# Performance work log

Hardware: AMD Instinct MI355X
Metric: run time of the kernel (lower is better)

## Reference

```python
import jax, jax.numpy as jnp
import numpy as np

T, B, D_IN = 1024, 64, 17
H_MAIN = 150   # per-direction hidden of main bi-GRU (hidden_dim=300)
H_HIER = 128   # per-direction hidden of hier bi-GRU (hier_hidden=256)
M = 16         # uniform measure length (eoM fires every M steps)
N_MEAS = T // M
N_PITCH, N_KS = 35, 15
PAD_P, PAD_K = 34, 14


def _gru(x, Wih, Whh, bih, bhh):
    # x: [T, N, D]; torch GRU gate order is (r, z, n)
    H = Whh.shape[1]
    gi_all = jnp.einsum('tnd,gd->tng', x, Wih) + bih  # input-side gates, precomputed

    def step(h, gi):
        gh = h @ Whh.T + bhh
        ir, iz, inn = jnp.split(gi, 3, axis=-1)
        hr, hz, hn = jnp.split(gh, 3, axis=-1)
        r = jax.nn.sigmoid(ir + hr)
        z = jax.nn.sigmoid(iz + hz)
        n = jnp.tanh(inn + r * hn)
        h_new = (1.0 - z) * n + z * h
        return h_new, h_new

    h0 = jnp.zeros((x.shape[1], H), x.dtype)
    _, ys = jax.lax.scan(step, h0, gi_all)
    return ys


def _bigru(x, pf, pb):
    yf = _gru(x, *pf)
    yb = _gru(x[::-1], *pb)[::-1]
    return jnp.concatenate([yf, yb], axis=-1)


def _ce(logits, targets, pad_idx):
    # mean cross-entropy with ignore_index=pad_idx
    logp = jax.nn.log_softmax(logits, axis=-1)
    mask = (targets != pad_idx).astype(logits.dtype)
    nll = -jnp.take_along_axis(logp, targets[:, None], axis=1)[:, 0]
    return jnp.sum(nll * mask) / jnp.maximum(jnp.sum(mask), 1.0)


def _forward(sentences, mWih_f, mWhh_f, mbih_f, mbhh_f, mWih_b, mWhh_b, mbih_b, mbhh_b,
             hWih_f, hWhh_f, hbih_f, hbhh_f, hWih_b, hWhh_b, hbih_b, hbhh_b,
             Wq, bq, Wv, bv, Wp, bp, Wk, bk, pitches, keysignatures):
    # main bi-GRU over full sequences: [T, B, 300]
    rnn_out = _bigru(sentences, (mWih_f, mWhh_f, mbih_f, mbhh_f),
                     (mWih_b, mWhh_b, mbih_b, mbhh_b))
    H2 = rnn_out.shape[-1]
    # carve uniform measures: [T,B,H2] -> [M, B*N_MEAS, H2]
    seg = rnn_out.reshape(N_MEAS, M, B, H2).transpose(1, 2, 0, 3).reshape(M, B * N_MEAS, H2)
    hier = _bigru(seg, (hWih_f, hWhh_f, hbih_f, hbhh_f),
                  (hWih_b, hWhh_b, hbih_b, hbhh_b))  # [M, B*N_MEAS, 256]
    HH = hier.shape[-1]
    # attention per measure: query = value = hier outputs [B*N_MEAS, M, 256]
    hv = hier.reshape(M, B, N_MEAS, HH).transpose(1, 2, 0, 3).reshape(B * N_MEAS, M, HH)
    q = hv @ Wq.T + bq
    v = hv @ Wv.T + bv
    attn = jax.nn.softmax(jnp.einsum('nld,nmd->nlm', q, v), axis=-1)
    ctx = jnp.einsum('nlm,nmd->nd', attn, hv).reshape(B, N_MEAS, HH)  # sum over l of attn@value
    # repeat each measure context over its M timesteps: [T, B, 256]
    ctx_t = jnp.repeat(ctx, M, axis=1).transpose(1, 0, 2)
    stacked = jnp.concatenate([rnn_out, ctx_t], axis=-1)  # [T, B, 556]
    out_pitch = stacked @ Wp.T + bp   # [T, B, 35]
    out_ks = ctx_t @ Wk.T + bk        # [T, B, 15]
    return (_ce(out_pitch.reshape(-1, N_PITCH), pitches.reshape(-1), PAD_P)
            + _ce(out_ks.reshape(-1, N_KS), keysignatures.reshape(-1), PAD_K))


def setup_inputs() -> dict:
    key = jax.random.key(0)
    ks = jax.random.split(key, 32)

    def w(i, *shape):
        return jax.random.normal(ks[i], shape, jnp.float32) * 0.05

    G_M, G_H = 3 * H_MAIN, 3 * H_HIER
    inp = {
        'sentences': jax.random.normal(ks[0], (T, B, D_IN), jnp.float32),
        'pitches': jax.random.randint(ks[1], (T, B), 0, PAD_P),
        'keysignatures': jax.random.randint(ks[2], (T, B), 0, PAD_K),
        'sentences_len': jnp.full((B,), T, dtype=jnp.int32),
        'eoM': jnp.tile(((jnp.arange(T) % M) == M - 1).astype(jnp.int32)[:, None], (1, B)),
        'mWih_f': w(3, G_M, D_IN), 'mWhh_f': w(4, G_M, H_MAIN), 'mbih_f': w(5, G_M), 'mbhh_f': w(6, G_M),
        'mWih_b': w(7, G_M, D_IN), 'mWhh_b': w(8, G_M, H_MAIN), 'mbih_b': w(9, G_M), 'mbhh_b': w(10, G_M),
        'hWih_f': w(11, G_H, 2 * H_MAIN), 'hWhh_f': w(12, G_H, H_HIER), 'hbih_f': w(13, G_H), 'hbhh_f': w(14, G_H),
        'hWih_b': w(15, G_H, 2 * H_MAIN), 'hWhh_b': w(16, G_H, H_HIER), 'hbih_b': w(17, G_H), 'hbhh_b': w(18, G_H),
        'Wq': w(19, 2 * H_HIER, 2 * H_HIER), 'bq': w(20, 2 * H_HIER),
        'Wv': w(21, 2 * H_HIER, 2 * H_HIER), 'bv': w(22, 2 * H_HIER),
        'Wp': w(23, N_PITCH, 2 * H_MAIN + 2 * H_HIER), 'bp': w(24, N_PITCH),
        'Wk': w(25, N_KS, 2 * H_HIER), 'bk': w(26, N_KS),
    }
    return inp


def reference(sentences, pitches, keysignatures, sentences_len, eoM,
              mWih_f, mWhh_f, mbih_f, mbhh_f, mWih_b, mWhh_b, mbih_b, mbhh_b,
              hWih_f, hWhh_f, hbih_f, hbhh_f, hWih_b, hWhh_b, hbih_b, hbhh_b,
              Wq, bq, Wv, bv, Wp, bp, Wk, bk):
    # sentences_len/eoM encode the (uniform) measure structure M=16, full lengths;
    # the segment layout is baked in statically, so they are structural constants here.
    return _forward(sentences, mWih_f, mWhh_f, mbih_f, mbhh_f, mWih_b, mWhh_b, mbih_b, mbhh_b,
                    hWih_f, hWhh_f, hbih_f, hbhh_f, hWih_b, hWhh_b, hbih_b, hbhh_b,
                    Wq, bq, Wv, bv, Wp, bp, Wk, bk, pitches, keysignatures)
```

## Files before the change

kernel.cpp:

```cpp
#include <hip/hip_runtime.h>
#include <cstddef>

constexpr int kT   = 1024;
constexpr int kB   = 64;
constexpr int kDIN = 17;
constexpr int kHM  = 150;
constexpr int kHH  = 128;
constexpr int kM   = 16;
constexpr int kD2  = 300;
constexpr int kNP  = 35;
constexpr int kNK  = 15;

constexpr size_t OFF_RNN16  = 0;
constexpr size_t OFF_HV16   = 10485760;
constexpr size_t OFF_PART   = 18894848;
constexpr size_t OFF_PTPACK = 19988480;
constexpr size_t OFF_U      = 20021248;
constexpr size_t OFF_W      = 20021504;
constexpr size_t OFF_C0     = 20021760;
constexpr size_t OFF_KSLOGP = 20021792;
constexpr size_t OFF_CLOG   = 20083232;
constexpr size_t OFF_BPACK  = 20318752;
constexpr size_t OFF_BPACKL = 20490784;

typedef __bf16 bf16x8 __attribute__((ext_vector_type(8)));
typedef float f32x4 __attribute__((ext_vector_type(4)));

__device__ __forceinline__ unsigned short f2bf(float f) {
  unsigned u = __float_as_uint(f);
  u += 0x7FFFu + ((u >> 16) & 1u);
  return (unsigned short)(u >> 16);
}
__device__ __forceinline__ float bf2f(unsigned short v) {
  return __uint_as_float(((unsigned)v) << 16);
}
__device__ __forceinline__ float sigm(float x) {
  return __builtin_amdgcn_rcpf(1.f + __expf(-x));
}
__device__ __forceinline__ float tanh_fast(float x) {
  return 1.f - 2.f * __builtin_amdgcn_rcpf(__expf(2.f * x) + 1.f);
}

__global__ __launch_bounds__(640, 2) void k_mega(
    const float* __restrict__ x,
    const float* __restrict__ mWih_f, const float* __restrict__ mWhh_f,
    const float* __restrict__ mWih_b, const float* __restrict__ mWhh_b,
    const float* __restrict__ mbih_f, const float* __restrict__ mbhh_f,
    const float* __restrict__ mbih_b, const float* __restrict__ mbhh_b,
    const float* __restrict__ hWih_f, const float* __restrict__ hWhh_f,
    const float* __restrict__ hWih_b, const float* __restrict__ hWhh_b,
    const float* __restrict__ Wp,
    const float* __restrict__ Wq, const float* __restrict__ bq,
    const float* __restrict__ Wv, const float* __restrict__ bv,
    unsigned short* __restrict__ rnn16,
    unsigned short* __restrict__ bpack,
    unsigned short* __restrict__ bpackL,
    unsigned short* __restrict__ pp,
    float* __restrict__ u, float* __restrict__ w,
    float* __restrict__ c0)
{
  __shared__ __align__(16) unsigned short hx[2][160];
  __shared__ __align__(16) unsigned short hist[2][16][160];
  __shared__ __align__(16) unsigned short xall[kT][32];
  const int blk = blockIdx.x;
  if (blk < 128) {
    const int d = blk & 1, b = blk >> 1;
    const int tid = threadIdx.x, wv = tid >> 6, lane = tid & 63;
    const int col = lane & 15, q8 = (lane >> 4) * 8;
    for (int i = tid; i < 2 * 160; i += 640) ((unsigned short*)hx)[i] = 0;
    for (int i = tid; i < 2 * 16 * 160; i += 640) ((unsigned short*)hist)[i] = 0;
    for (int i = tid; i < kT * 32; i += 640) {
      const int t = i >> 5, c = i & 31;
      xall[t][c] = (c < kDIN) ? f2bf(x[((size_t)t * kB + b) * kDIN + c])
                              : (unsigned short)0;
    }
    const float* bih = d ? mbih_b : mbih_f;
    const float* bhh = d ? mbhh_b : mbhh_f;
    const float* Wihd = d ? mWih_b : mWih_f;
    const float* Whhd = d ? mWhh_b : mWhh_f;
    const int j = wv * 16 + col;
    const bool actv = (lane < 16) && (j < kHM);
    float br = 0.f, bz = 0.f, bnx = 0.f, bnh = 0.f;
    if (actv) {
      br  = bih[j] + bhh[j];
      bz  = bih[150 + j] + bhh[150 + j];
      bnx = bih[300 + j];
      bnh = bhh[300 + j];
    }
    bf16x8 bw[3][6];
    const int gts[3] = { wv, 10 + wv, 20 + wv };
    const int kb = (lane >> 4) * 8;
#pragma unroll
    for (int gi = 0; gi < 3; gi++) {
      const int slot = gts[gi] * 16 + col;
      const int type = slot / 160, jh = slot - type * 160;
      const int row = type * 150 + jh;
      const bool valid = (jh < 150);
#pragma unroll
      for (int kt = 0; kt < 6; kt++) {
        union { bf16x8 v; unsigned short us[8]; } tmp;
        if (kt < 5) {
          const int k0 = kt * 32 + kb;
          if (valid && (k0 + 8 <= 150)) {
#pragma unroll
            for (int p = 0; p < 4; p++) {
              const float2 f2 = *(const float2*)&Whhd[row * 150 + k0 + 2 * p];
              tmp.us[2 * p]     = f2bf(f2.x);
              tmp.us[2 * p + 1] = f2bf(f2.y);
            }
          } else {
#pragma unroll
            for (int jj = 0; jj < 8; jj++) {
              const int k = k0 + jj;
              tmp.us[jj] = (valid && k < 150) ? f2bf(Whhd[row * 150 + k])
                                              : (unsigned short)0;
            }
          }
        } else {
#pragma unroll
          for (int jj = 0; jj < 8; jj++) {
            const int k = kb + jj;
            tmp.us[jj] = (valid && k < 17) ? f2bf(Wihd[row * 17 + k])
                                           : (unsigned short)0;
          }
        }
        bw[gi][kt] = tmp.v;
      }
    }
    float h_old = 0.f;
    __syncthreads();

    for (int t = 0; t < kT; t++) {
      const int tx = d ? (kT - 1 - t) : t;
      const int buf = t & 1;
      bf16x8 afr[6];
#pragma unroll
      for (int kt = 0; kt < 5; kt++) afr[kt] = *(const bf16x8*)&hx[buf][kt * 32 + q8];
      afr[5] = *(const bf16x8*)&xall[tx][q8];
      f32x4 aR0 = (f32x4)(0.f), aR1 = (f32x4)(0.f), aR2 = (f32x4)(0.f);
      f32x4 aZ0 = (f32x4)(0.f), aZ1 = (f32x4)(0.f), aZ2 = (f32x4)(0.f);
      f32x4 aN0 = (f32x4)(0.f), aN1 = (f32x4)(0.f), aN2 = (f32x4)(0.f);
      f32x4 aX  = (f32x4)(0.f);
      aR0 = __builtin_amdgcn_mfma_f32_16x16x32_bf16(afr[0], bw[0][0], aR0, 0, 0, 0);
      aZ0 = __builtin_amdgcn_mfma_f32_16x16x32_bf16(afr[0], bw[1][0], aZ0, 0, 0, 0);
      aN0 = __builtin_amdgcn_mfma_f32_16x16x32_bf16(afr[0], bw[2][0], aN0, 0, 0, 0);
      aR1 = __builtin_amdgcn_mfma_f32_16x16x32_bf16(afr[1], bw[0][1], aR1, 0, 0, 0);
      aZ1 = __builtin_amdgcn_mfma_f32_16x16x32_bf16(afr[1], bw[1][1], aZ1, 0, 0, 0);
      aN1 = __builtin_amdgcn_mfma_f32_16x16x32_bf16(afr[1], bw[2][1], aN1, 0, 0, 0);
      aR2 = __builtin_amdgcn_mfma_f32_16x16x32_bf16(afr[2], bw[0][2], aR2, 0, 0, 0);
      aZ2 = __builtin_amdgcn_mfma_f32_16x16x32_bf16(afr[2], bw[1][2], aZ2, 0, 0, 0);
      aN2 = __builtin_amdgcn_mfma_f32_16x16x32_bf16(afr[2], bw[2][2], aN2, 0, 0, 0);
      aR0 = __builtin_amdgcn_mfma_f32_16x16x32_bf16(afr[3], bw[0][3], aR0, 0, 0, 0);
      aZ0 = __builtin_amdgcn_mfma_f32_16x16x32_bf16(afr[3], bw[1][3], aZ0, 0, 0, 0);
      aN0 = __builtin_amdgcn_mfma_f32_16x16x32_bf16(afr[3], bw[2][3], aN0, 0, 0, 0);
      aR1 = __builtin_amdgcn_mfma_f32_16x16x32_bf16(afr[4], bw[0][4], aR1, 0, 0, 0);
      aZ1 = __builtin_amdgcn_mfma_f32_16x16x32_bf16(afr[4], bw[1][4], aZ1, 0, 0, 0);
      aN1 = __builtin_amdgcn_mfma_f32_16x16x32_bf16(afr[4], bw[2][4], aN1, 0, 0, 0);
      aR2 = __builtin_amdgcn_mfma_f32_16x16x32_bf16(afr[5], bw[0][5], aR2, 0, 0, 0);
      aZ2 = __builtin_amdgcn_mfma_f32_16x16x32_bf16(afr[5], bw[1][5], aZ2, 0, 0, 0);
      aX  = __builtin_amdgcn_mfma_f32_16x16x32_bf16(afr[5], bw[2][5], aX, 0, 0, 0);
      if (actv) {
        const float r = sigm(aR0[0] + aR1[0] + aR2[0] + br);
        const float z = sigm(aZ0[0] + aZ1[0] + aZ2[0] + bz);
        const float n = tanh_fast(aX[0] + bnx + r * (aN0[0] + aN1[0] + aN2[0] + bnh));
        h_old = (1.f - z) * n + z * h_old;
        const unsigned short us = f2bf(h_old);
        hx[buf ^ 1][j] = us;
        hist[(t >> 4) & 1][t & 15][j] = us;
      }
      __syncthreads();
      if ((t & 15) == 15) {
        const int hb = (t >> 4) & 1;
        const int toff = tid / 40, ch = tid - toff * 40;
        const int tg = t - 15 + toff;
        const int txg = d ? (kT - 1 - tg) : tg;
        *(ushort4*)&rnn16[((size_t)txg * kB + b) * 320 + d * 160 + ch * 4] =
            *(const ushort4*)&hist[hb][toff][ch * 4];
      }
    }
  } else if (blk < 199) {
    const int sub = threadIdx.x >> 6, lane = threadIdx.x & 63;
    int bid = (blk - 128) * 10 + sub;
    if (bid >= 702) return;
    if (bid < 672) {
      const int kt = bid % 14;
      const int nt = (bid / 14) % 24;
      const int d  = bid / (14 * 24);
      const float* Wih = d ? hWih_b : hWih_f;
      const float* Whh = d ? hWhh_b : hWhh_f;
      const int n = nt * 16 + (lane & 15);
      const int kbase = kt * 32 + (lane >> 4) * 8;
      unsigned short* dst = bpack + ((((size_t)d * 24 + nt) * 14 + kt) * 64 + lane) * 8;
#pragma unroll
      for (int jj = 0; jj < 8; jj++) {
        const int k = kbase + jj;
        float f = 0.f;
        if (kt < 10) {
          if (k < 150) f = Wih[n * 300 + k];
          else if (k >= 160 && k < 310) f = Wih[n * 300 + (k - 10)];
        } else {
          f = Whh[n * 128 + (k - 320)];
        }
        dst[jj] = f2bf(f);
      }
    } else {
      bid -= 672;
      const int kt = bid % 10, nt = bid / 10;
      const int n = nt * 16 + (lane & 15);
      const int kbase = kt * 32 + (lane >> 4) * 8;
      unsigned short* dst = bpackL + (((size_t)bid) * 64 + lane) * 8;
#pragma unroll
      for (int jj = 0; jj < 8; jj++) {
        const int k = kbase + jj;
        float f = 0.f;
        if (n < kNP) {
          if (k < 150) f = Wp[n * 556 + k];
          else if (k >= 160 && k < 310) f = Wp[n * 556 + (k - 10)];
        }
        dst[jj] = f2bf(f);
      }
    }
  } else if (blk < 212) {
    const int sub = threadIdx.x >> 6, lane = threadIdx.x & 63;
    const int bid = (blk - 199) * 10 + sub;
    if (bid >= 128) return;
    const int kt = bid & 7, nt = bid >> 3;
    const int c = nt * 16 + (lane & 15);
    const int e0 = kt * 32 + (lane >> 4) * 8;
    float av[8];
#pragma unroll
    for (int jj = 0; jj < 8; jj++) av[jj] = 0.f;
    for (int a = 0; a < 256; a++) {
      const float wq = Wq[a * 256 + c];
#pragma unroll
      for (int jj = 0; jj < 8; jj++) av[jj] += wq * Wv[a * 256 + e0 + jj];
    }
    unsigned short* dst = pp + ((size_t)bid * 64 + lane) * 8;
#pragma unroll
    for (int jj = 0; jj < 8; jj++) dst[jj] = f2bf(av[jj]);
  } else {
    const int a = threadIdx.x;
    if (a >= 256) return;
    float us = 0.f, ws = 0.f;
    for (int jj = 0; jj < 256; jj++) {
      us += Wq[jj * 256 + a] * bv[jj];
      ws += bq[jj] * Wv[jj * 256 + a];
    }
    u[a] = us; w[a] = ws;
    if (a == 0) {
      float cc = 0.f;
      for (int jj = 0; jj < 256; jj++) cc += bq[jj] * bv[jj];
      c0[0] = cc;
    }
  }
}

__global__ __launch_bounds__(512, 1) void k_hier_mfma(
    const unsigned short* __restrict__ rnn16,
    const unsigned short* __restrict__ bpack,
    const float* __restrict__ bihf, const float* __restrict__ bhhf,
    const float* __restrict__ bihb, const float* __restrict__ bhhb,
    unsigned short* __restrict__ hv16)
{
  const int d = blockIdx.x & 1;
  const int bn0 = (blockIdx.x >> 1) * 16;
  const int tid = threadIdx.x;
  const int w = tid >> 6;
  const int lane = tid & 63;
  const int q = lane >> 4, col = lane & 15, q8 = q * 8;

  __shared__ __align__(16) unsigned short x_s[2][16][328];
  __shared__ __align__(16) unsigned short h_s[16][136];

  for (int i = tid; i < 16 * 136; i += 512) ((unsigned short*)h_s)[i] = 0;
  const float* bih = d ? bihb : bihf;
  const float* bhh = d ? bhhb : bhhf;
  const int j = w * 16 + col;
  const float biR  = bih[j] + bhh[j];
  const float biZ  = bih[128 + j] + bhh[128 + j];
  const float biNX = bih[256 + j];
  const float biNH = bhh[256 + j];
  float h32r[4] = {0.f, 0.f, 0.f, 0.f};

  bf16x8 bw[3][14];
  const unsigned short* bpd = bpack + (size_t)d * 24 * 14 * 64 * 8;
  const int nts[3] = { w, 8 + w, 16 + w };
#pragma unroll
  for (int gi = 0; gi < 3; gi++)
#pragma unroll
    for (int kt = 0; kt < 14; kt++)
      bw[gi][kt] = *(const bf16x8*)&bpd[(((size_t)nts[gi] * 14 + kt) * 64 + lane) * 8];

  const int i0 = tid,        r0 = i0 / 40, c0 = i0 - r0 * 40;
  const int i1 = tid + 512,  r1 = i1 / 40, c1 = i1 - r1 * 40;
  const int bnA = bn0 + r0, bbA = bnA >> 6, nnA = bnA & 63;
  const int bnB = bn0 + r1, bbB = bnB >> 6, nnB = bnB & 63;

  {
    const int mx0 = d ? 15 : 0;
    *(uint4*)&x_s[0][r0][c0 * 8] =
        *(const uint4*)&rnn16[((size_t)(nnA * 16 + mx0) * 64 + bbA) * 320 + c0 * 8];
    if (tid < 128)
      *(uint4*)&x_s[0][r1][c1 * 8] =
          *(const uint4*)&rnn16[((size_t)(nnB * 16 + mx0) * 64 + bbB) * 320 + c1 * 8];
  }
  __syncthreads();

  for (int m = 0; m < kM; m++) {
    const int mx = d ? (15 - m) : m;
    const int buf = m & 1;
    uint4 pf0, pf1;
    const bool has = (m + 1 < kM);
    if (has) {
      const int mxn = d ? (15 - (m + 1)) : (m + 1);
      pf0 = *(const uint4*)&rnn16[((size_t)(nnA * 16 + mxn) * 64 + bbA) * 320 + c0 * 8];
      if (tid < 128)
        pf1 = *(const uint4*)&rnn16[((size_t)(nnB * 16 + mxn) * 64 + bbB) * 320 + c1 * 8];
    }
    f32x4 aR = (f32x4)(0.f), aZ = (f32x4)(0.f), aNX = (f32x4)(0.f), aNH = (f32x4)(0.f);
#pragma unroll
    for (int kt = 0; kt < 14; kt++) {
      const bf16x8 af = (kt < 10) ? *(const bf16x8*)&x_s[buf][col][kt * 32 + q8]
                                  : *(const bf16x8*)&h_s[col][(kt - 10) * 32 + q8];
      aR = __builtin_amdgcn_mfma_f32_16x16x32_bf16(af, bw[0][kt], aR, 0, 0, 0);
      aZ = __builtin_amdgcn_mfma_f32_16x16x32_bf16(af, bw[1][kt], aZ, 0, 0, 0);
      if (kt < 10) aNX = __builtin_amdgcn_mfma_f32_16x16x32_bf16(af, bw[2][kt], aNX, 0, 0, 0);
      else         aNH = __builtin_amdgcn_mfma_f32_16x16x32_bf16(af, bw[2][kt], aNH, 0, 0, 0);
    }
    __syncthreads();
#pragma unroll
    for (int i = 0; i < 4; i++) {
      const int row = q * 4 + i;
      const float rr = sigm(aR[i] + biR);
      const float zz = sigm(aZ[i] + biZ);
      const float nn2 = tanh_fast(aNX[i] + biNX + rr * (aNH[i] + biNH));
      const float hnew = (1.f - zz) * nn2 + zz * h32r[i];
      h32r[i] = hnew;
      const unsigned short us = f2bf(hnew);
      h_s[row][j] = us;
      hv16[((size_t)(bn0 + row) * kM + mx) * 256 + d * kHH + j] = us;
    }
    if (has) {
      *(uint4*)&x_s[buf ^ 1][r0][c0 * 8] = pf0;
      if (tid < 128) *(uint4*)&x_s[buf ^ 1][r1][c1 * 8] = pf1;
    }
    __syncthreads();
  }
}

__global__ __launch_bounds__(256) void k_attn_ctx(
    const unsigned short* __restrict__ hv16, const unsigned short* __restrict__ ptpack,
    const float* __restrict__ u, const float* __restrict__ w,
    const float* __restrict__ c0p,
    const float* __restrict__ Wp, const float* __restrict__ bp,
    const float* __restrict__ Wk, const float* __restrict__ bk,
    float* __restrict__ clog, float* __restrict__ kslogp) {
  const int tid = threadIdx.x;
  const int wv = tid >> 6, lane = tid & 63, col = lane & 15, q = lane >> 4, q8 = q * 8;
  __shared__ __align__(16) unsigned short hv16s[16][264];
  __shared__ __align__(16) unsigned short Ts16[16][264];
  __shared__ __align__(16) float W2[50][260];
  __shared__ __align__(16) float cs[256];
  __shared__ __align__(16) float us[256], wss[256];
  __shared__ float pu[16][17], pw[16][17];
  __shared__ float uh[16], wh[16], SM[16];
  __shared__ float As[16][17];
  __shared__ float arr[64];
  __shared__ float bps[35], bks[15];
  const float c0 = c0p[0];
  for (int i = tid; i < 35 * 256; i += 256) { const int r = i >> 8, c = i & 255; W2[r][c] = Wp[r * 556 + 300 + c]; }
  for (int i = tid; i < 15 * 256; i += 256) { const int r = i >> 8, c = i & 255; W2[35 + r][c] = Wk[r * 256 + c]; }
  us[tid] = u[tid];
  wss[tid] = w[tid];
  if (tid < 35) bps[tid] = bp[tid];
  else if (tid < 50) bks[tid - 35] = bk[tid - 35];
  bf16x8 bpt[4][8];
#pragma unroll
  for (int i2 = 0; i2 < 4; i2++)
#pragma unroll
    for (int kt = 0; kt < 8; kt++)
      bpt[i2][kt] = *(const bf16x8*)&ptpack[((((size_t)(wv * 4 + i2)) * 8 + kt) * 64 + lane) * 8];

  const int srow = tid >> 4, sci = (tid & 15) * 16;
  {
    const unsigned short* src = hv16 + (size_t)(blockIdx.x * 8) * 4096;
#pragma unroll
    for (int k = 0; k < 16; k += 4)
      *(ushort4*)&hv16s[srow][sci + k] = *(const ushort4*)&src[srow * 256 + sci + k];
  }
  __syncthreads();

  for (int ni = 0; ni < 8; ni++) {
    const int n = blockIdx.x * 8 + ni;
    ushort4 pf[4];
    if (ni + 1 < 8) {
      const unsigned short* src = hv16 + (size_t)(n + 1) * 4096;
#pragma unroll
      for (int k2 = 0; k2 < 4; k2++) pf[k2] = *(const ushort4*)&src[srow * 256 + sci + k2 * 4];
    }
    {
      f32x4 acc4[4];
#pragma unroll
      for (int i2 = 0; i2 < 4; i2++) acc4[i2] = (f32x4)(0.f);
#pragma unroll
      for (int kt = 0; kt < 8; kt++) {
        const bf16x8 af = *(const bf16x8*)&hv16s[col][kt * 32 + q8];
#pragma unroll
        for (int i2 = 0; i2 < 4; i2++)
          acc4[i2] = __builtin_amdgcn_mfma_f32_16x16x32_bf16(af, bpt[i2][kt], acc4[i2], 0, 0, 0);
      }
#pragma unroll
      for (int i2 = 0; i2 < 4; i2++) {
        const int nt = wv * 4 + i2;
#pragma unroll
        for (int i = 0; i < 4; i++) Ts16[q * 4 + i][nt * 16 + col] = f2bf(acc4[i2][i]);
      }
    }
    {
      const int l = tid >> 4, s = tid & 15;
      float su = 0.f, sw = 0.f;
#pragma unroll
      for (int a0 = 0; a0 < 16; a0++) {
        const int a = s * 16 + a0;
        const float hvv = bf2f(hv16s[l][a]);
        su += hvv * us[a];
        sw += hvv * wss[a];
      }
      pu[l][s] = su; pw[l][s] = sw;
    }
    __syncthreads();
    if (tid < 16) { float s2 = 0.f; for (int s = 0; s < 16; s++) s2 += pu[tid][s]; uh[tid] = s2; }
    else if (tid < 32) { float s2 = 0.f; for (int s = 0; s < 16; s++) s2 += pw[tid - 16][s]; wh[tid - 16] = s2; }
    __syncthreads();
    if (tid < 64) {
      f32x4 sa = (f32x4)(0.f);
#pragma unroll
      for (int kt = 0; kt < 8; kt++) {
        const bf16x8 af  = *(const bf16x8*)&hv16s[col][kt * 32 + q8];
        const bf16x8 bts = *(const bf16x8*)&Ts16[col][kt * 32 + q8];
        sa = __builtin_amdgcn_mfma_f32_16x16x32_bf16(af, bts, sa, 0, 0, 0);
      }
#pragma unroll
      for (int i = 0; i < 4; i++) {
        const int l = q * 4 + i;
        float sc = sa[i] + c0 + uh[l] + wh[col];
        float mxv = sc;
#pragma unroll
        for (int o = 8; o >= 1; o >>= 1) mxv = fmaxf(mxv, __shfl_xor(mxv, o, 16));
        const float e = __expf(sc - mxv);
        float se = e;
#pragma unroll
        for (int o = 8; o >= 1; o >>= 1) se += __shfl_xor(se, o, 16);
        As[l][col] = e / se;
      }
    }
    __syncthreads();
    if (tid < 16) {
      float s = 0.f;
      for (int l2 = 0; l2 < 16; l2++) s += As[l2][tid];
      SM[tid] = s;
    }
    __syncthreads();
    {
      float cv = 0.f;
#pragma unroll
      for (int m2 = 0; m2 < 16; m2++) cv += SM[m2] * bf2f(hv16s[m2][tid]);
      cs[tid] = cv;
    }
    __syncthreads();
    if (ni + 1 < 8) {
#pragma unroll
      for (int k2 = 0; k2 < 4; k2++) *(ushort4*)&hv16s[srow][sci + k2 * 4] = pf[k2];
    }
    {
      const int o = tid >> 2, s = tid & 3;
      float v = 0.f;
      if (o < 50) {
        for (int k0 = 0; k0 < 64; k0 += 4) {
          const int k = s * 64 + k0;
          const float4 wq = *(const float4*)&W2[o][k];
          const float4 cq = *(const float4*)&cs[k];
          v += wq.x * cq.x + wq.y * cq.y + wq.z * cq.z + wq.w * cq.w;
        }
      }
      v += __shfl_xor(v, 1);
      v += __shfl_xor(v, 2);
      if (o < 50 && s == 0) arr[o] = v;
    }
    __syncthreads();
    if (tid < 35) clog[n * kNP + tid] = arr[tid] + bps[tid];
    if (tid >= 64 && tid < 80) {
      const int t2 = tid - 64;
      float kk = (t2 < 15) ? arr[35 + t2] + bks[t2] : -1e30f;
      float mxv = kk;
#pragma unroll
      for (int off = 8; off >= 1; off >>= 1) mxv = fmaxf(mxv, __shfl_xor(mxv, off, 16));
      const float e = (t2 < 15) ? __expf(kk - mxv) : 0.f;
      float se = e;
#pragma unroll
      for (int off = 8; off >= 1; off >>= 1) se += __shfl_xor(se, off, 16);
      if (t2 < 15) kslogp[n * kNK + t2] = kk - mxv - __logf(se);
    }
    __syncthreads();
  }
}

__global__ __launch_bounds__(256, 2) void k_loss_mfma(
    const unsigned short* __restrict__ rnn16,
    const unsigned short* __restrict__ bpackL,
    const float* __restrict__ clog,
    const float* __restrict__ ks_logp,
    const int* __restrict__ pitches, const int* __restrict__ kss,
    float4* __restrict__ partial) {
  const int tid = threadIdx.x, w = tid >> 6, lane = tid & 63;
  const int col = lane & 15, q = lane >> 4, q8 = q * 8;
  __shared__ __align__(16) unsigned short xls[64][328];
  __shared__ float red[4][4];
  bf16x8 bl[3][10];
#pragma unroll
  for (int nt = 0; nt < 3; nt++)
#pragma unroll
    for (int kt = 0; kt < 10; kt++)
      bl[nt][kt] = *(const bf16x8*)&bpackL[(((size_t)nt * 10 + kt) * 64 + lane) * 8];

  {
    const size_t base = (size_t)blockIdx.x * 64;
    for (int i = tid; i < 64 * 40; i += 256) {
      const int r = i / 40, c = i - r * 40;
      *(uint4*)&xls[r][c * 8] = *(const uint4*)&rnn16[(base + r) * 320 + c * 8];
    }
  }
  __syncthreads();

  float sp = 0.f, cp = 0.f, sk = 0.f, ck = 0.f;
  {
    const int rowbase = blockIdx.x * 64 + w * 16;
    f32x4 a0 = (f32x4)(0.f), a1 = (f32x4)(0.f), a2 = (f32x4)(0.f);
#pragma unroll
    for (int kt = 0; kt < 10; kt++) {
      const bf16x8 af = *(const bf16x8*)&xls[w * 16 + col][kt * 32 + q8];
      a0 = __builtin_amdgcn_mfma_f32_16x16x32_bf16(af, bl[0][kt], a0, 0, 0, 0);
      a1 = __builtin_amdgcn_mfma_f32_16x16x32_bf16(af, bl[1][kt], a1, 0, 0, 0);
      a2 = __builtin_amdgcn_mfma_f32_16x16x32_bf16(af, bl[2][kt], a2, 0, 0, 0);
    }
#pragma unroll
    for (int i = 0; i < 4; i++) {
      const int row = rowbase + q * 4 + i;
      const int t = row >> 6, b = row & 63;
      const int bn = b * 64 + (t >> 4);
      const float lg0 = a0[i] + clog[bn * kNP + col];
      const float lg1 = a1[i] + clog[bn * kNP + 16 + col];
      const float lg2 = (col < 3) ? (a2[i] + clog[bn * kNP + 32 + col]) : -1e30f;
      float mx = fmaxf(fmaxf(lg0, lg1), lg2);
#pragma unroll
      for (int o = 8; o >= 1; o >>= 1) mx = fmaxf(mx, __shfl_xor(mx, o, 16));
      float se = __expf(lg0 - mx) + __expf(lg1 - mx) + __expf(lg2 - mx);
#pragma unroll
      for (int o = 8; o >= 1; o >>= 1) se += __shfl_xor(se, o, 16);
      const int tp = pitches[row];
      const float cand = (tp < 16) ? a0[i] : (tp < 32) ? a1[i] : a2[i];
      const float tva = __shfl(cand, (lane & 48) | (tp & 15), 64);
      if (col == 0 && tp != 34) {
        sp += (mx + __logf(se)) - (tva + clog[bn * kNP + tp]);
        cp += 1.f;
      }
      if (col == 1) {
        const int tk = kss[row];
        if (tk != 14) { sk -= ks_logp[bn * kNK + tk]; ck += 1.f; }
      }
    }
  }
#pragma unroll
  for (int o = 32; o >= 1; o >>= 1) {
    sp += __shfl_xor(sp, o, 64);
    cp += __shfl_xor(cp, o, 64);
    sk += __shfl_xor(sk, o, 64);
    ck += __shfl_xor(ck, o, 64);
  }
  if (lane == 0) { red[w][0] = sp; red[w][1] = cp; red[w][2] = sk; red[w][3] = ck; }
  __syncthreads();
  if (tid == 0) {
    float p0 = 0.f, p1 = 0.f, p2 = 0.f, p3 = 0.f;
#pragma unroll
    for (int q2 = 0; q2 < 4; q2++) { p0 += red[q2][0]; p1 += red[q2][1]; p2 += red[q2][2]; p3 += red[q2][3]; }
    partial[blockIdx.x] = make_float4(p0, p1, p2, p3);
  }
}

__global__ __launch_bounds__(256) void k_final(const float4* __restrict__ partial,
                                               float* __restrict__ out) {
  const int tid = threadIdx.x, w = tid >> 6, lane = tid & 63;
  __shared__ float4 red[4];
  float s0 = 0.f, s1 = 0.f, s2 = 0.f, s3 = 0.f;
#pragma unroll
  for (int k = 0; k < 4; k++) {
    const float4 p = partial[tid + 256 * k];
    s0 += p.x; s1 += p.y; s2 += p.z; s3 += p.w;
  }
#pragma unroll
  for (int o = 32; o >= 1; o >>= 1) {
    s0 += __shfl_xor(s0, o, 64);
    s1 += __shfl_xor(s1, o, 64);
    s2 += __shfl_xor(s2, o, 64);
    s3 += __shfl_xor(s3, o, 64);
  }
  if (lane == 0) red[w] = make_float4(s0, s1, s2, s3);
  __syncthreads();
  if (tid == 0) {
    float a0 = 0.f, a1 = 0.f, a2 = 0.f, a3 = 0.f;
#pragma unroll
    for (int q = 0; q < 4; q++) { a0 += red[q].x; a1 += red[q].y; a2 += red[q].z; a3 += red[q].w; }
    out[0] = a0 / fmaxf(a1, 1.f) + a2 / fmaxf(a3, 1.f);
  }
}

extern "C" void kernel_launch(void* const* d_in, const int* in_sizes, int n_in,
                              void* d_out, int out_size, void* d_ws, size_t ws_size,
                              hipStream_t stream) {
  (void)in_sizes; (void)n_in; (void)out_size; (void)ws_size;
  const float* sent    = (const float*)d_in[0];
  const int*   pitches = (const int*)d_in[1];
  const int*   kss     = (const int*)d_in[2];
  const float* mWih_f  = (const float*)d_in[5];
  const float* mWhh_f  = (const float*)d_in[6];
  const float* mbih_f  = (const float*)d_in[7];
  const float* mbhh_f  = (const float*)d_in[8];
  const float* mWih_b  = (const float*)d_in[9];
  const float* mWhh_b  = (const float*)d_in[10];
  const float* mbih_b  = (const float*)d_in[11];
  const float* mbhh_b  = (const float*)d_in[12];
  const float* hWih_f  = (const float*)d_in[13];
  const float* hWhh_f  = (const float*)d_in[14];
  const float* hbih_f  = (const float*)d_in[15];
  const float* hbhh_f  = (const float*)d_in[16];
  const float* hWih_b  = (const float*)d_in[17];
  const float* hWhh_b  = (const float*)d_in[18];
  const float* hbih_b  = (const float*)d_in[19];
  const float* hbhh_b  = (const float*)d_in[20];
  const float* Wq      = (const float*)d_in[21];
  const float* bq      = (const float*)d_in[22];
  const float* Wv      = (const float*)d_in[23];
  const float* bv      = (const float*)d_in[24];
  const float* Wp      = (const float*)d_in[25];
  const float* bp      = (const float*)d_in[26];
  const float* Wk      = (const float*)d_in[27];
  const float* bk      = (const float*)d_in[28];
  float* ws  = (float*)d_ws;
  float* out = (float*)d_out;
  unsigned short* rnn16  = (unsigned short*)(ws + OFF_RNN16);
  unsigned short* hv16   = (unsigned short*)(ws + OFF_HV16);
  unsigned short* ptpack = (unsigned short*)(ws + OFF_PTPACK);
  unsigned short* bpackL = (unsigned short*)(ws + OFF_BPACKL);
  unsigned short* bpack  = (unsigned short*)(ws + OFF_BPACK);
  float4* partial = (float4*)(ws + OFF_PART);

  k_mega<<<213, 640, 0, stream>>>(sent,
                                  mWih_f, mWhh_f, mWih_b, mWhh_b,
                                  mbih_f, mbhh_f, mbih_b, mbhh_b,
                                  hWih_f, hWhh_f, hWih_b, hWhh_b, Wp,
                                  Wq, bq, Wv, bv,
                                  rnn16, bpack, bpackL, ptpack,
                                  ws + OFF_U, ws + OFF_W, ws + OFF_C0);
  k_hier_mfma<<<512, 512, 0, stream>>>(rnn16, bpack,
                                       hbih_f, hbhh_f, hbih_b, hbhh_b, hv16);
  k_attn_ctx<<<512, 256, 0, stream>>>(hv16, ptpack, ws + OFF_U, ws + OFF_W,
                                      ws + OFF_C0, Wp, bp, Wk, bk,
                                      ws + OFF_CLOG, ws + OFF_KSLOGP);
  k_loss_mfma<<<1024, 256, 0, stream>>>(rnn16, bpackL, ws + OFF_CLOG, ws + OFF_KSLOGP,
                                        pitches, kss, partial);
  k_final<<<1, 256, 0, stream>>>(partial, out);
}
```

Before: 910.8 us.

## Batch 16 sequences per block in main GRU recurrence using full MFMA rows

The main bi-GRU recurrence previously used one block per (batch, direction) and fed a single sequence through 16-row MFMAs, so 15 of 16 rows were wasted. Now each of 8 blocks processes 16 batch rows at once, with 5 waves each covering two 16-column tiles per gate. Hidden states are kept in an 8-slot LDS ring and flushed to global memory every 8 steps, and inputs are prefetched one chunk ahead into a double buffer. This cuts total MFMA work and block count, but leaves only 8 blocks doing the serial 1024-step chain, so each step carries twice the MFMA work per wave and a barrier; the weight-packing block ranges are remapped to the smaller block size.

```diff
diff --git a/kernel.cpp b/kernel.cpp
--- a/kernel.cpp
+++ b/kernel.cpp
@@ -7,7 +7,6 @@
 constexpr int kHM  = 150;
 constexpr int kHH  = 128;
 constexpr int kM   = 16;
-constexpr int kD2  = 300;
 constexpr int kNP  = 35;
 constexpr int kNK  = 15;
 
@@ -41,7 +40,7 @@
   return 1.f - 2.f * __builtin_amdgcn_rcpf(__expf(2.f * x) + 1.f);
 }
 
-__global__ __launch_bounds__(640, 2) void k_mega(
+__global__ __launch_bounds__(320, 1) void k_mega(
     const float* __restrict__ x,
     const float* __restrict__ mWih_f, const float* __restrict__ mWhh_f,
     const float* __restrict__ mWih_b, const float* __restrict__ mWhh_b,
@@ -59,39 +58,39 @@
     float* __restrict__ u, float* __restrict__ w,
     float* __restrict__ c0)
 {
-  __shared__ __align__(16) unsigned short hx[2][160];
-  __shared__ __align__(16) unsigned short hist[2][16][160];
-  __shared__ __align__(16) unsigned short xall[kT][32];
+  __shared__ __align__(16) unsigned short hring[8][16][168];
+  __shared__ __align__(16) unsigned short xring[2][8][16][40];
   const int blk = blockIdx.x;
-  if (blk < 128) {
-    const int d = blk & 1, b = blk >> 1;
+  if (blk < 8) {
+    const int d = blk >> 2, b0 = (blk & 3) * 16;
     const int tid = threadIdx.x, wv = tid >> 6, lane = tid & 63;
-    const int col = lane & 15, q8 = (lane >> 4) * 8;
-    for (int i = tid; i < 2 * 160; i += 640) ((unsigned short*)hx)[i] = 0;
-    for (int i = tid; i < 2 * 16 * 160; i += 640) ((unsigned short*)hist)[i] = 0;
-    for (int i = tid; i < kT * 32; i += 640) {
-      const int t = i >> 5, c = i & 31;
-      xall[t][c] = (c < kDIN) ? f2bf(x[((size_t)t * kB + b) * kDIN + c])
-                              : (unsigned short)0;
-    }
+    const int col = lane & 15, q = lane >> 4, q8 = q * 8;
+    for (int i = tid; i < 8 * 16 * 168; i += 320) ((unsigned short*)hring)[i] = 0;
+    for (int i = tid; i < 2 * 8 * 16 * 40; i += 320) ((unsigned short*)xring)[i] = 0;
+
     const float* bih = d ? mbih_b : mbih_f;
     const float* bhh = d ? mbhh_b : mbhh_f;
     const float* Wihd = d ? mWih_b : mWih_f;
     const float* Whhd = d ? mWhh_b : mWhh_f;
-    const int j = wv * 16 + col;
-    const bool actv = (lane < 16) && (j < kHM);
-    float br = 0.f, bz = 0.f, bnx = 0.f, bnh = 0.f;
-    if (actv) {
-      br  = bih[j] + bhh[j];
-      bz  = bih[150 + j] + bhh[150 + j];
-      bnx = bih[300 + j];
-      bnh = bhh[300 + j];
-    }
-    bf16x8 bw[3][6];
-    const int gts[3] = { wv, 10 + wv, 20 + wv };
-    const int kb = (lane >> 4) * 8;
-#pragma unroll
-    for (int gi = 0; gi < 3; gi++) {
+    const int j0 = 32 * wv + col;
+    const int j1 = j0 + 16;
+    const float br0 = bih[j0] + bhh[j0];
+    const float bz0 = bih[150 + j0] + bhh[150 + j0];
+    const float bnx0 = bih[300 + j0];
+    const float bnh0 = bhh[300 + j0];
+    float br1 = 0.f, bz1 = 0.f, bnx1 = 0.f, bnh1 = 0.f;
+    if (j1 < kHM) {
+      br1 = bih[j1] + bhh[j1];
+      bz1 = bih[150 + j1] + bhh[150 + j1];
+      bnx1 = bih[300 + j1];
+      bnh1 = bhh[300 + j1];
+    }
+    bf16x8 bw[6][6];
+    const int gts[6] = { 2 * wv, 2 * wv + 1, 10 + 2 * wv, 11 + 2 * wv,
+                         20 + 2 * wv, 21 + 2 * wv };
+    const int kb = q * 8;
+#pragma unroll
+    for (int gi = 0; gi < 6; gi++) {
       const int slot = gts[gi] * 16 + col;
       const int type = slot / 160, jh = slot - type * 160;
       const int row = type * 150 + jh;
@@ -127,60 +126,106 @@
         bw[gi][kt] = tmp.v;
       }
     }
-    float h_old = 0.f;
-    __syncthreads();
-
-    for (int t = 0; t < kT; t++) {
-      const int tx = d ? (kT - 1 - t) : t;
-      const int buf = t & 1;
-      bf16x8 afr[6];
-#pragma unroll
-      for (int kt = 0; kt < 5; kt++) afr[kt] = *(const bf16x8*)&hx[buf][kt * 32 + q8];
-      afr[5] = *(const bf16x8*)&xall[tx][q8];
-      f32x4 aR0 = (f32x4)(0.f), aR1 = (f32x4)(0.f), aR2 = (f32x4)(0.f);
-      f32x4 aZ0 = (f32x4)(0.f), aZ1 = (f32x4)(0.f), aZ2 = (f32x4)(0.f);
-      f32x4 aN0 = (f32x4)(0.f), aN1 = (f32x4)(0.f), aN2 = (f32x4)(0.f);
-      f32x4 aX  = (f32x4)(0.f);
-      aR0 = __builtin_amdgcn_mfma_f32_16x16x32_bf16(afr[0], bw[0][0], aR0, 0, 0, 0);
-      aZ0 = __builtin_amdgcn_mfma_f32_16x16x32_bf16(afr[0], bw[1][0], aZ0, 0, 0, 0);
-      aN0 = __builtin_amdgcn_mfma_f32_16x16x32_bf16(afr[0], bw[2][0], aN0, 0, 0, 0);
-      aR1 = __builtin_amdgcn_mfma_f32_16x16x32_bf16(afr[1], bw[0][1], aR1, 0, 0, 0);
-      aZ1 = __builtin_amdgcn_mfma_f32_16x16x32_bf16(afr[1], bw[1][1], aZ1, 0, 0, 0);
-      aN1 = __builtin_amdgcn_mfma_f32_16x16x32_bf16(afr[1], bw[2][1], aN1, 0, 0, 0);
-      aR2 = __builtin_amdgcn_mfma_f32_16x16x32_bf16(afr[2], bw[0][2], aR2, 0, 0, 0);
-      aZ2 = __builtin_amdgcn_mfma_f32_16x16x32_bf16(afr[2], bw[1][2], aZ2, 0, 0, 0);
-      aN2 = __builtin_amdgcn_mfma_f32_16x16x32_bf16(afr[2], bw[2][2], aN2, 0, 0, 0);
-      aR0 = __builtin_amdgcn_mfma_f32_16x16x32_bf16(afr[3], bw[0][3], aR0, 0, 0, 0);
-      aZ0 = __builtin_amdgcn_mfma_f32_16x16x32_bf16(afr[3], bw[1][3], aZ0, 0, 0, 0);
-      aN0 = __builtin_amdgcn_mfma_f32_16x16x32_bf16(afr[3], bw[2][3], aN0, 0, 0, 0);
-      aR1 = __builtin_amdgcn_mfma_f32_16x16x32_bf16(afr[4], bw[0][4], aR1, 0, 0, 0);
-      aZ1 = __builtin_amdgcn_mfma_f32_16x16x32_bf16(afr[4], bw[1][4], aZ1, 0, 0, 0);
-      aN1 = __builtin_amdgcn_mfma_f32_16x16x32_bf16(afr[4], bw[2][4], aN1, 0, 0, 0);
-      aR2 = __builtin_amdgcn_mfma_f32_16x16x32_bf16(afr[5], bw[0][5], aR2, 0, 0, 0);
-      aZ2 = __builtin_amdgcn_mfma_f32_16x16x32_bf16(afr[5], bw[1][5], aZ2, 0, 0, 0);
-      aX  = __builtin_amdgcn_mfma_f32_16x16x32_bf16(afr[5], bw[2][5], aX, 0, 0, 0);
-      if (actv) {
-        const float r = sigm(aR0[0] + aR1[0] + aR2[0] + br);
-        const float z = sigm(aZ0[0] + aZ1[0] + aZ2[0] + bz);
-        const float n = tanh_fast(aX[0] + bnx + r * (aN0[0] + aN1[0] + aN2[0] + bnh));
-        h_old = (1.f - z) * n + z * h_old;
-        const unsigned short us = f2bf(h_old);
-        hx[buf ^ 1][j] = us;
-        hist[(t >> 4) & 1][t & 15][j] = us;
+    const int flrow = tid / 20, flch = tid - flrow * 20;
+    float h_old[2][4] = {{0.f,0.f,0.f,0.f},{0.f,0.f,0.f,0.f}};
+    __syncthreads();
+    {
+      for (int it = 0; it < 7; it++) {
+        const int idx = it * 320 + tid;
+        if (idx < 2176) {
+          const int trel = idx / 272, rem = idx - trel * 272;
+          const int bb = rem / 17, cc = rem - bb * 17;
+          const int tt = trel;
+          const int tx = d ? (1023 - tt) : tt;
+          xring[0][trel][bb][cc] = f2bf(x[((size_t)tx * kB + b0 + bb) * kDIN + cc]);
+        }
+      }
+    }
+    __syncthreads();
+
+    for (int s = 0; s < 128; s++) {
+      const int t0 = s * 8;
+      float xpf[7];
+      const bool haspf = (s + 1 < 128);
+      if (haspf) {
+#pragma unroll
+        for (int it = 0; it < 7; it++) {
+          const int idx = it * 320 + tid;
+          if (idx < 2176) {
+            const int trel = idx / 272, rem = idx - trel * 272;
+            const int bb = rem / 17, cc = rem - bb * 17;
+            const int tt = t0 + 8 + trel;
+            const int tx = d ? (1023 - tt) : tt;
+            xpf[it] = x[((size_t)tx * kB + b0 + bb) * kDIN + cc];
+          }
+        }
+      }
+      for (int tt = 0; tt < 8; tt++) {
+        const int t = t0 + tt;
+        const int sprev = (t + 7) & 7;
+        bf16x8 ah[5];
+#pragma unroll
+        for (int kt = 0; kt < 5; kt++)
+          ah[kt] = *(const bf16x8*)&hring[sprev][col][kt * 32 + q8];
+        const bf16x8 ax = *(const bf16x8*)&xring[s & 1][tt][col][q8];
+        f32x4 aR[2], aZ[2], aNh[2], aNx[2];
+#pragma unroll
+        for (int jt = 0; jt < 2; jt++) {
+          aR[jt] = (f32x4)(0.f); aZ[jt] = (f32x4)(0.f);
+          aNh[jt] = (f32x4)(0.f); aNx[jt] = (f32x4)(0.f);
+        }
+#pragma unroll
+        for (int jt = 0; jt < 2; jt++) {
+#pragma unroll
+          for (int kt = 0; kt < 5; kt++) {
+            aR[jt]  = __builtin_amdgcn_mfma_f32_16x16x32_bf16(ah[kt], bw[0 + jt][kt], aR[jt], 0, 0, 0);
+            aZ[jt]  = __builtin_amdgcn_mfma_f32_16x16x32_bf16(ah[kt], bw[2 + jt][kt], aZ[jt], 0, 0, 0);
+            aNh[jt] = __builtin_amdgcn_mfma_f32_16x16x32_bf16(ah[kt], bw[4 + jt][kt], aNh[jt], 0, 0, 0);
+          }
+          aR[jt]  = __builtin_amdgcn_mfma_f32_16x16x32_bf16(ax, bw[0 + jt][5], aR[jt], 0, 0, 0);
+          aZ[jt]  = __builtin_amdgcn_mfma_f32_16x16x32_bf16(ax, bw[2 + jt][5], aZ[jt], 0, 0, 0);
+          aNx[jt] = __builtin_amdgcn_mfma_f32_16x16x32_bf16(ax, bw[4 + jt][5], aNx[jt], 0, 0, 0);
+        }
+        const int snew = t & 7;
+#pragma unroll
+        for (int jt = 0; jt < 2; jt++) {
+          const int j = jt ? j1 : j0;
+          const float brv = jt ? br1 : br0, bzv = jt ? bz1 : bz0;
+          const float bnxv = jt ? bnx1 : bnx0, bnhv = jt ? bnh1 : bnh0;
+#pragma unroll
+          for (int i = 0; i < 4; i++) {
+            const int row = q * 4 + i;
+            const float r = sigm(aR[jt][i] + brv);
+            const float z = sigm(aZ[jt][i] + bzv);
+            const float n = tanh_fast(aNx[jt][i] + bnxv + r * (aNh[jt][i] + bnhv));
+            h_old[jt][i] = (1.f - z) * n + z * h_old[jt][i];
+            hring[snew][row][j] = f2bf(h_old[jt][i]);
+          }
+        }
+        __syncthreads();
+      }
+      for (int s2 = 0; s2 < 8; s2++) {
+        const int tg = t0 + s2;
+        const int txg = d ? (1023 - tg) : tg;
+        *(uint4*)&rnn16[((size_t)txg * kB + b0 + flrow) * 320 + d * 160 + flch * 8] =
+            *(const uint4*)&hring[s2][flrow][flch * 8];
+      }
+      if (haspf) {
+#pragma unroll
+        for (int it = 0; it < 7; it++) {
+          const int idx = it * 320 + tid;
+          if (idx < 2176) {
+            const int trel = idx / 272, rem = idx - trel * 272;
+            const int bb = rem / 17, cc = rem - bb * 17;
+            xring[(s + 1) & 1][trel][bb][cc] = f2bf(xpf[it]);
+          }
+        }
       }
       __syncthreads();
-      if ((t & 15) == 15) {
-        const int hb = (t >> 4) & 1;
-        const int toff = tid / 40, ch = tid - toff * 40;
-        const int tg = t - 15 + toff;
-        const int txg = d ? (kT - 1 - tg) : tg;
-        *(ushort4*)&rnn16[((size_t)txg * kB + b) * 320 + d * 160 + ch * 4] =
-            *(const ushort4*)&hist[hb][toff][ch * 4];
-      }
-    }
-  } else if (blk < 199) {
+    }
+  } else if (blk < 149) {
     const int sub = threadIdx.x >> 6, lane = threadIdx.x & 63;
-    int bid = (blk - 128) * 10 + sub;
+    int bid = (blk - 8) * 5 + sub;
     if (bid >= 702) return;
     if (bid < 672) {
       const int kt = bid % 14;
@@ -220,9 +265,9 @@
         dst[jj] = f2bf(f);
       }
     }
-  } else if (blk < 212) {
+  } else if (blk < 175) {
     const int sub = threadIdx.x >> 6, lane = threadIdx.x & 63;
-    const int bid = (blk - 199) * 10 + sub;
+    const int bid = (blk - 149) * 5 + sub;
     if (bid >= 128) return;
     const int kt = bid & 7, nt = bid >> 3;
     const int c = nt * 16 + (lane & 15);
@@ -654,7 +699,7 @@
   unsigned short* bpack  = (unsigned short*)(ws + OFF_BPACK);
   float4* partial = (float4*)(ws + OFF_PART);
 
-  k_mega<<<213, 640, 0, stream>>>(sent,
+  k_mega<<<176, 320, 0, stream>>>(sent,
                                   mWih_f, mWhh_f, mWih_b, mWhh_b,
                                   mbih_f, mbhh_f, mbih_b, mbhh_b,
                                   hWih_f, hWhh_f, hWih_b, hWhh_b, Wp,
```

Result: slower. 1.768 ms (+94.1%).
